# Optimization experiments

Measured on AMD Instinct MI355X. Metric: run time of the kernel, lower is better.

Reference implementation:

```python
import jax, jax.numpy as jnp
import numpy as np

B, H, S, D, KG = 1, 8, 1024, 64, 10

def setup_inputs() -> dict:
    key = jax.random.key(0)
    ks = jax.random.split(key, 16)
    n = jax.random.normal
    u = jax.random.uniform
    return {
        'Q': n(ks[0], (B, H, S, D), dtype=jnp.float32),
        'K': n(ks[1], (B, H, S, D), dtype=jnp.float32),
        'V': n(ks[2], (B, H, S, D), dtype=jnp.float32),
        'distance_matrix': u(ks[3], (B, H, S, S), dtype=jnp.float32) * 10.0,
        'energy_matrix': u(ks[4], (B, H, S, S), dtype=jnp.float32) * 5.0,
        'mask': jnp.ones((B, H, S, S), dtype=jnp.int32),
        'mu_D': n(ks[5], (KG,), dtype=jnp.float32),
        'sigma_D': u(ks[6], (KG,), dtype=jnp.float32) + 0.5,  # keep sigma positive
        'b_D': n(ks[7], (KG,), dtype=jnp.float32) * 0.1,
        'mu_E': n(ks[8], (KG,), dtype=jnp.float32),
        'sigma_E': u(ks[9], (KG,), dtype=jnp.float32) + 0.5,
        'b_E': n(ks[10], (KG,), dtype=jnp.float32) * 0.1,
        'W1': n(ks[11], (KG, KG), dtype=jnp.float32) / np.sqrt(KG),
        'b1': jnp.zeros((KG,), dtype=jnp.float32),
        'W2': n(ks[12], (1, KG), dtype=jnp.float32) / np.sqrt(KG),
        'b2': jnp.zeros((1,), dtype=jnp.float32),
    }


def _rbf_mlp_bias(x, b, mu, sigma, W1, b1, W2, b2):
    # x: [B,H,S,S] -> Gaussian RBF features over K kernels, then small MLP -> [B,H,S,S]
    z = (x[..., None] + b - mu) / sigma                      # [B,H,S,S,K]
    inv_norm = 1.0 / (jnp.sqrt(2.0 * jnp.pi) * sigma)
    psi = jnp.exp(-0.5 * z * z) * inv_norm                   # [B,H,S,S,K]
    h = jax.nn.gelu(jnp.einsum('bhijk,lk->bhijl', psi, W1) + b1, approximate=False)
    return (jnp.einsum('bhijk,lk->bhijl', h, W2) + b2)[..., 0]


def reference(Q, K, V, distance_matrix, energy_matrix, mask,
              mu_D, sigma_D, b_D, mu_E, sigma_E, b_E, W1, b1, W2, b2):
    d_model = Q.shape[-1]
    scores = jnp.einsum('bhid,bhjd->bhij', Q, K) / np.sqrt(d_model * 2)
    scores = scores + _rbf_mlp_bias(distance_matrix, b_D, mu_D, sigma_D, W1, b1, W2, b2)
    scores = scores + _rbf_mlp_bias(energy_matrix, b_E, mu_E, sigma_E, W1, b1, W2, b2)
    scores = jnp.where(mask == 0, jnp.float32(-1e9), scores)
    attn = jax.nn.softmax(scores, axis=-1)
    return jnp.einsum('bhij,bhjd->bhid', attn, V)
```

## Files before the change

kernel.cpp:

```cpp
#include <hip/hip_runtime.h>
#include <math.h>

#define Hn 8
#define Sn 1024
#define Dn 64
#define KG 10

#define TN 2048
#define RD 10.25f
#define RE 5.125f

typedef __attribute__((ext_vector_type(8))) short bf16x8;
typedef __attribute__((ext_vector_type(4))) float f32x4;
typedef _Float16 f16;
typedef __attribute__((ext_vector_type(8))) _Float16 f16x8;
typedef unsigned short u16;
typedef unsigned int u32;

__device__ inline float bf2f(u16 u) {
    union { u32 i; float f; } v;
    v.i = ((u32)u) << 16;
    return v.f;
}

__device__ inline u16 f2bf(float f) {
    union { float f; u32 i; } v;
    v.f = f;
    u32 i = v.i;
    return (u16)((i + 0x7FFFu + ((i >> 16) & 1u)) >> 16);
}

__device__ float bias_eval(float x,
                           const float* __restrict__ mu, const float* __restrict__ sg,
                           const float* __restrict__ bb,
                           const float* __restrict__ W1, const float* __restrict__ b1,
                           const float* __restrict__ W2, const float* __restrict__ b2) {
    const float inv_s2pi = 0.39894228040143267794f;
    float psi[KG];
#pragma unroll
    for (int k = 0; k < KG; k++) {
        float s = sg[k];
        float z = (x + bb[k] - mu[k]) / s;
        psi[k] = __expf(-0.5f * z * z) * (inv_s2pi / s);
    }
    float out = b2[0];
#pragma unroll
    for (int l = 0; l < KG; l++) {
        float a = b1[l];
#pragma unroll
        for (int k = 0; k < KG; k++) a += psi[k] * W1[l * KG + k];
        float g = 0.5f * a * (1.0f + erff(a * 0.70710678118654752440f));
        out += g * W2[l];
    }
    return out;
}

#define QK4 262144
#define VTN 524288

__global__ __launch_bounds__(256) void prep_kernel(
    const float* __restrict__ Q, const float* __restrict__ K, const float* __restrict__ V,
    const float* __restrict__ muD, const float* __restrict__ sgD, const float* __restrict__ bD,
    const float* __restrict__ muE, const float* __restrict__ sgE, const float* __restrict__ bE,
    const float* __restrict__ W1, const float* __restrict__ b1,
    const float* __restrict__ W2, const float* __restrict__ b2,
    u32* __restrict__ tab, u16* __restrict__ Qb, u16* __restrict__ Kb, u16* __restrict__ VTi)
{
    int id = blockIdx.x * 256 + threadIdx.x;
    if (id < 2 * TN) {
        int which = (id >= TN);
        int idx = id & (TN - 1);
        float h = (which ? RE : RD) / (float)TN;
        float x0 = idx * h;
        float v0, v1;
        if (which) {
            v0 = bias_eval(x0,     muE, sgE, bE, W1, b1, W2, b2);
            v1 = bias_eval(x0 + h, muE, sgE, bE, W1, b1, W2, b2);
        } else {
            v0 = bias_eval(x0,     muD, sgD, bD, W1, b1, W2, b2);
            v1 = bias_eval(x0 + h, muD, sgD, bD, W1, b1, W2, b2);
        }
        tab[id] = (u32)f2bf(v0) | ((u32)f2bf(v1 - v0) << 16);
    } else if (id < 2 * TN + QK4) {
        int i = id - 2 * TN;
        int arr = i >> 17;
        i &= (1 << 17) - 1;
        float4 v = ((const float4*)(arr ? K : Q))[i];
        ushort4 o;
        o.x = f2bf(v.x); o.y = f2bf(v.y); o.z = f2bf(v.z); o.w = f2bf(v.w);
        ((ushort4*)(arr ? Kb : Qb))[i] = o;
    } else if (id < 2 * TN + QK4 + VTN) {
        int g = id - (2 * TN + QK4);
        int h = g >> 16;
        int d = (g >> 10) & 63;
        int s = g & 1023;
        int t = s >> 5, q = (s >> 3) & 3, j = s & 7;
        int src_s = (t << 5) + (q << 2) + (j & 3) + ((j >> 2) << 4);
        VTi[g] = f2bf(V[(((size_t)h << 10) + src_s) * Dn + d]);
    }
}

__device__ inline float lerp_tab(const u32* __restrict__ st, float x, float invh) {
    float tf = x * invh;
    int i = (int)tf;
    i = max(0, min(i, TN - 1));
    float fr = tf - (float)i;
    u32 p = st[i];
    return fmaf(bf2f((u16)(p >> 16)), fr, bf2f((u16)p));
}

#define CB_GROUPS (Hn * 64 * 4 * 8 * 64)

__global__ __launch_bounds__(256) void bias_kernel(
    const float* __restrict__ Dm, const float* __restrict__ Em, const int* __restrict__ Mk,
    const u32* __restrict__ gtab, f16* __restrict__ Cb)
{
    __shared__ __align__(16) u32 sTab[2 * TN];
    const int tid = threadIdx.x;
    {
        const uint4* g4 = (const uint4*)gtab;
        uint4* s4 = (uint4*)sTab;
#pragma unroll
        for (int i = 0; i < 4; i++) s4[tid + 256 * i] = g4[tid + 256 * i];
    }
    __syncthreads();
    const float invhD = (float)TN / RD;
    const float invhE = (float)TN / RE;

    for (int g = blockIdx.x * 256 + tid; g < CB_GROUPS; g += gridDim.x * 256) {
        const int lane = g & 63;
        const int t    = (g >> 6) & 7;
        const int w    = (g >> 9) & 3;
        const int qb   = (g >> 11) & 63;
        const int h    = g >> 17;
        const int q    = qb * 16 + (lane & 15);
        const int k    = w * 256 + t * 32 + (lane >> 4) * 4;
        const size_t base = ((((size_t)h << 10) + q) << 10) + k;

        const float4 d0 = *(const float4*)(Dm + base);
        const float4 d1 = *(const float4*)(Dm + base + 16);
        const float4 e0 = *(const float4*)(Em + base);
        const float4 e1 = *(const float4*)(Em + base + 16);
        const int4   m0 = *(const int4*)(Mk + base);
        const int4   m1 = *(const int4*)(Mk + base + 16);

        const float dv[8] = {d0.x, d0.y, d0.z, d0.w, d1.x, d1.y, d1.z, d1.w};
        const float ev[8] = {e0.x, e0.y, e0.z, e0.w, e1.x, e1.y, e1.z, e1.w};
        const int   mv[8] = {m0.x, m0.y, m0.z, m0.w, m1.x, m1.y, m1.z, m1.w};

        f16x8 o;
#pragma unroll
        for (int j = 0; j < 8; j++) {
            float b = lerp_tab(sTab, dv[j], invhD) + lerp_tab(sTab + TN, ev[j], invhE);
            o[j] = (f16)((mv[j] == 0) ? -60000.0f : b);
        }
        ((f16x8*)Cb)[g] = o;
    }
}

__global__ __launch_bounds__(256) void attn_kernel(
    const u16* __restrict__ Qb, const u16* __restrict__ Kb, const u16* __restrict__ VTi,
    const f16* __restrict__ Cb, float* __restrict__ out)
{
    __shared__ float sO[4][16][68];
    __shared__ float sM[4][16], sL[4][16];

    const int tid  = threadIdx.x;
    const int h    = blockIdx.y;
    const int qb   = blockIdx.x;
    const int q0   = qb * 16;
    const int wave = tid >> 6;
    const int lane = tid & 63;
    const int quad = lane >> 4;
    const int l16  = lane & 15;

    const u16* Qh = Qb  + (size_t)h * Sn * Dn;
    const u16* Kh = Kb  + (size_t)h * Sn * Dn;
    const u16* Vh = VTi + (size_t)h * Dn * Sn;
    const f16x8* Cw = (const f16x8*)Cb
                    + (size_t)(((h * 64 + qb) * 4 + wave) * 8) * 64 + lane;
    const float scale = 0.08838834764831845f;

    const bf16x8 bQ0 = *(const bf16x8*)(Qh + (q0 + l16) * Dn + quad * 8);
    const bf16x8 bQ1 = *(const bf16x8*)(Qh + (q0 + l16) * Dn + 32 + quad * 8);

    f32x4 O0 = {0.f, 0.f, 0.f, 0.f}, O1 = O0, O2 = O0, O3 = O0;
    float m_run = -1e30f, l_run = 0.f;

    bf16x8 Ka[2][4];
    bf16x8 Va[2][4];
    f16x8  Ca[2];

#define LOADT(buf, tt) do {                                                   \
        const int k0_ = wave * 256 + (tt) * 32;                               \
        const u16* kr_ = Kh + (size_t)(k0_ + l16) * Dn + quad * 8;            \
        Ka[buf][0] = *(const bf16x8*)(kr_);                                   \
        Ka[buf][1] = *(const bf16x8*)(kr_ + 32);                              \
        Ka[buf][2] = *(const bf16x8*)(kr_ + 16 * Dn);                         \
        Ka[buf][3] = *(const bf16x8*)(kr_ + 16 * Dn + 32);                    \
        const u16* vr_ = Vh + k0_ + quad * 8 + (size_t)l16 * Sn;              \
        Va[buf][0] = *(const bf16x8*)(vr_);                                   \
        Va[buf][1] = *(const bf16x8*)(vr_ + 16 * Sn);                         \
        Va[buf][2] = *(const bf16x8*)(vr_ + 32 * Sn);                         \
        Va[buf][3] = *(const bf16x8*)(vr_ + 48 * Sn);                         \
        Ca[buf]    = Cw[(tt) * 64];                                           \
    } while (0)

    LOADT(0, 0);

#pragma unroll
    for (int t = 0; t < 8; t++) {
        const int cur = t & 1;
        if (t < 7) LOADT(cur ^ 1, t + 1);

        f32x4 s0 = {0.f, 0.f, 0.f, 0.f}, s1 = s0;
        s0 = __builtin_amdgcn_mfma_f32_16x16x32_bf16(Ka[cur][0], bQ0, s0, 0, 0, 0);
        s0 = __builtin_amdgcn_mfma_f32_16x16x32_bf16(Ka[cur][1], bQ1, s0, 0, 0, 0);
        s1 = __builtin_amdgcn_mfma_f32_16x16x32_bf16(Ka[cur][2], bQ0, s1, 0, 0, 0);
        s1 = __builtin_amdgcn_mfma_f32_16x16x32_bf16(Ka[cur][3], bQ1, s1, 0, 0, 0);

        float sc0[4], sc1[4];
#pragma unroll
        for (int r = 0; r < 4; r++) {
            sc0[r] = fmaf(s0[r], scale, (float)Ca[cur][r]);
            sc1[r] = fmaf(s1[r], scale, (float)Ca[cur][4 + r]);
        }

        float mloc = fmaxf(fmaxf(fmaxf(sc0[0], sc0[1]), fmaxf(sc0[2], sc0[3])),
                           fmaxf(fmaxf(sc1[0], sc1[1]), fmaxf(sc1[2], sc1[3])));
        mloc = fmaxf(mloc, __shfl_xor(mloc, 16, 64));
        mloc = fmaxf(mloc, __shfl_xor(mloc, 32, 64));

        const float mn = fmaxf(m_run, mloc);
        const float al = __expf(m_run - mn);
        m_run = mn;

        float p0[4], p1[4], ll = 0.f;
#pragma unroll
        for (int r = 0; r < 4; r++) {
            p0[r] = __expf(sc0[r] - mn);
            p1[r] = __expf(sc1[r] - mn);
            ll += p0[r] + p1[r];
        }
        ll += __shfl_xor(ll, 16, 64);
        ll += __shfl_xor(ll, 32, 64);
        l_run = l_run * al + ll;

        bf16x8 aP;
#pragma unroll
        for (int r = 0; r < 4; r++) {
            aP[r]     = (short)f2bf(p0[r]);
            aP[4 + r] = (short)f2bf(p1[r]);
        }

        const float a0 = __shfl(al, quad * 4 + 0, 64);
        const float a1 = __shfl(al, quad * 4 + 1, 64);
        const float a2 = __shfl(al, quad * 4 + 2, 64);
        const float a3 = __shfl(al, quad * 4 + 3, 64);
        O0[0] *= a0; O0[1] *= a1; O0[2] *= a2; O0[3] *= a3;
        O1[0] *= a0; O1[1] *= a1; O1[2] *= a2; O1[3] *= a3;
        O2[0] *= a0; O2[1] *= a1; O2[2] *= a2; O2[3] *= a3;
        O3[0] *= a0; O3[1] *= a1; O3[2] *= a2; O3[3] *= a3;

        O0 = __builtin_amdgcn_mfma_f32_16x16x32_bf16(aP, Va[cur][0], O0, 0, 0, 0);
        O1 = __builtin_amdgcn_mfma_f32_16x16x32_bf16(aP, Va[cur][1], O1, 0, 0, 0);
        O2 = __builtin_amdgcn_mfma_f32_16x16x32_bf16(aP, Va[cur][2], O2, 0, 0, 0);
        O3 = __builtin_amdgcn_mfma_f32_16x16x32_bf16(aP, Va[cur][3], O3, 0, 0, 0);
    }
#undef LOADT

    if (lane < 16) {
        sM[wave][lane] = m_run;
        sL[wave][lane] = l_run;
    }
#pragma unroll
    for (int r = 0; r < 4; r++) {
        sO[wave][quad * 4 + r][ 0 + l16] = O0[r];
        sO[wave][quad * 4 + r][16 + l16] = O1[r];
        sO[wave][quad * 4 + r][32 + l16] = O2[r];
        sO[wave][quad * 4 + r][48 + l16] = O3[r];
    }
    __syncthreads();

    const int row = tid >> 4;
    const int c4  = (tid & 15) * 4;
    float mg = sM[0][row];
#pragma unroll
    for (int w = 1; w < 4; w++) mg = fmaxf(mg, sM[w][row]);
    float fac[4], lg = 0.f;
#pragma unroll
    for (int w = 0; w < 4; w++) {
        fac[w] = __expf(sM[w][row] - mg);
        lg += sL[w][row] * fac[w];
    }
    const float inv = 1.0f / lg;

    float acc[4];
#pragma unroll
    for (int c = 0; c < 4; c++) {
        acc[c] = 0.f;
#pragma unroll
        for (int w = 0; w < 4; w++) acc[c] += sO[w][row][c4 + c] * fac[w];
        acc[c] *= inv;
    }
    float4 ov = {acc[0], acc[1], acc[2], acc[3]};
    *(float4*)(out + ((size_t)(h * Sn + q0 + row)) * Dn + c4) = ov;
}

extern "C" void kernel_launch(void* const* d_in, const int* in_sizes, int n_in,
                              void* d_out, int out_size, void* d_ws, size_t ws_size,
                              hipStream_t stream) {
    const float* Q    = (const float*)d_in[0];
    const float* K    = (const float*)d_in[1];
    const float* V    = (const float*)d_in[2];
    const float* Dm   = (const float*)d_in[3];
    const float* Em   = (const float*)d_in[4];
    const int*   Mask = (const int*)d_in[5];
    const float* muD  = (const float*)d_in[6];
    const float* sgD  = (const float*)d_in[7];
    const float* bD   = (const float*)d_in[8];
    const float* muE  = (const float*)d_in[9];
    const float* sgE  = (const float*)d_in[10];
    const float* bE   = (const float*)d_in[11];
    const float* W1   = (const float*)d_in[12];
    const float* b1   = (const float*)d_in[13];
    const float* W2   = (const float*)d_in[14];
    const float* b2   = (const float*)d_in[15];

    u32* tab = (u32*)d_ws;
    u16* Qb  = (u16*)((char*)d_ws + 2 * TN * 4);
    u16* Kb  = Qb + (size_t)Hn * Sn * Dn;
    u16* VTi = Kb + (size_t)Hn * Sn * Dn;
    f16* Cb  = (f16*)(VTi + (size_t)Hn * Sn * Dn);

    const int prep_threads = 2 * TN + QK4 + VTN;
    prep_kernel<<<prep_threads / 256, 256, 0, stream>>>(
        Q, K, V, muD, sgD, bD, muE, sgE, bE, W1, b1, W2, b2,
        tab, Qb, Kb, VTi);

    bias_kernel<<<2048, 256, 0, stream>>>(Dm, Em, Mask, tab, Cb);

    dim3 grid(Sn / 16, Hn);
    attn_kernel<<<grid, 256, 0, stream>>>(Qb, Kb, VTi, Cb, (float*)d_out);
}
```

Before: 185.4 us.

## Stage K/V tiles via global_load_lds and store bias in natural row-major layout

The bias kernel now writes the combined bias in plain row-major [h][q][k] order instead of an MFMA-fragment-swizzled layout, so its reads and writes are contiguous. The attention kernel drops the register double-buffered K/V/bias prefetch and instead stages each K/V tile straight into LDS with global_load_lds, waiting on vmcnt(0) before reading it back. Bias is read as two f16x4 loads per row. The intent is to cut register pressure and get coalesced traffic, but the software pipelining goes away, so each iteration waits on its own loads and memory latency is exposed.

```diff
diff --git a/kernel.cpp b/kernel.cpp
--- a/kernel.cpp
+++ b/kernel.cpp
@@ -13,6 +13,7 @@
 typedef __attribute__((ext_vector_type(8))) short bf16x8;
 typedef __attribute__((ext_vector_type(4))) float f32x4;
 typedef _Float16 f16;
+typedef __attribute__((ext_vector_type(4))) _Float16 f16x4;
 typedef __attribute__((ext_vector_type(8))) _Float16 f16x8;
 typedef unsigned short u16;
 typedef unsigned int u32;
@@ -28,6 +29,13 @@
     v.f = f;
     u32 i = v.i;
     return (u16)((i + 0x7FFFu + ((i >> 16) & 1u)) >> 16);
+}
+
+__device__ inline void stage16(const void* g, void* l) {
+    __builtin_amdgcn_global_load_lds(
+        (const __attribute__((address_space(1))) unsigned int*)g,
+        (__attribute__((address_space(3))) unsigned int*)l,
+        16, 0, 0);
 }
 
 __device__ float bias_eval(float x,
@@ -109,7 +117,7 @@
     return fmaf(bf2f((u16)(p >> 16)), fr, bf2f((u16)p));
 }
 
-#define CB_GROUPS (Hn * 64 * 4 * 8 * 64)
+#define CB_GROUPS (Hn * Sn * Sn / 8)
 
 __global__ __launch_bounds__(256) void bias_kernel(
     const float* __restrict__ Dm, const float* __restrict__ Em, const int* __restrict__ Mk,
@@ -128,21 +136,14 @@
     const float invhE = (float)TN / RE;
 
     for (int g = blockIdx.x * 256 + tid; g < CB_GROUPS; g += gridDim.x * 256) {
-        const int lane = g & 63;
-        const int t    = (g >> 6) & 7;
-        const int w    = (g >> 9) & 3;
-        const int qb   = (g >> 11) & 63;
-        const int h    = g >> 17;
-        const int q    = qb * 16 + (lane & 15);
-        const int k    = w * 256 + t * 32 + (lane >> 4) * 4;
-        const size_t base = ((((size_t)h << 10) + q) << 10) + k;
+        const size_t base = (size_t)g * 8;
 
         const float4 d0 = *(const float4*)(Dm + base);
-        const float4 d1 = *(const float4*)(Dm + base + 16);
+        const float4 d1 = *(const float4*)(Dm + base + 4);
         const float4 e0 = *(const float4*)(Em + base);
-        const float4 e1 = *(const float4*)(Em + base + 16);
+        const float4 e1 = *(const float4*)(Em + base + 4);
         const int4   m0 = *(const int4*)(Mk + base);
-        const int4   m1 = *(const int4*)(Mk + base + 16);
+        const int4   m1 = *(const int4*)(Mk + base + 4);
 
         const float dv[8] = {d0.x, d0.y, d0.z, d0.w, d1.x, d1.y, d1.z, d1.w};
         const float ev[8] = {e0.x, e0.y, e0.z, e0.w, e1.x, e1.y, e1.z, e1.w};
@@ -162,13 +163,12 @@
     const u16* __restrict__ Qb, const u16* __restrict__ Kb, const u16* __restrict__ VTi,
     const f16* __restrict__ Cb, float* __restrict__ out)
 {
-    __shared__ float sO[4][16][68];
+    __shared__ __align__(16) char sBuf[4 * 8 * 1024];
     __shared__ float sM[4][16], sL[4][16];
 
     const int tid  = threadIdx.x;
     const int h    = blockIdx.y;
-    const int qb   = blockIdx.x;
-    const int q0   = qb * 16;
+    const int q0   = blockIdx.x * 16;
     const int wave = tid >> 6;
     const int lane = tid & 63;
     const int quad = lane >> 4;
@@ -177,53 +177,57 @@
     const u16* Qh = Qb  + (size_t)h * Sn * Dn;
     const u16* Kh = Kb  + (size_t)h * Sn * Dn;
     const u16* Vh = VTi + (size_t)h * Dn * Sn;
-    const f16x8* Cw = (const f16x8*)Cb
-                    + (size_t)(((h * 64 + qb) * 4 + wave) * 8) * 64 + lane;
+    const f16* Ch = Cb  + ((size_t)h * Sn + (q0 + l16)) * Sn;
     const float scale = 0.08838834764831845f;
 
     const bf16x8 bQ0 = *(const bf16x8*)(Qh + (q0 + l16) * Dn + quad * 8);
     const bf16x8 bQ1 = *(const bf16x8*)(Qh + (q0 + l16) * Dn + 32 + quad * 8);
 
+    char* st = sBuf + wave * 8192;
+
     f32x4 O0 = {0.f, 0.f, 0.f, 0.f}, O1 = O0, O2 = O0, O3 = O0;
     float m_run = -1e30f, l_run = 0.f;
 
-    bf16x8 Ka[2][4];
-    bf16x8 Va[2][4];
-    f16x8  Ca[2];
-
-#define LOADT(buf, tt) do {                                                   \
-        const int k0_ = wave * 256 + (tt) * 32;                               \
-        const u16* kr_ = Kh + (size_t)(k0_ + l16) * Dn + quad * 8;            \
-        Ka[buf][0] = *(const bf16x8*)(kr_);                                   \
-        Ka[buf][1] = *(const bf16x8*)(kr_ + 32);                              \
-        Ka[buf][2] = *(const bf16x8*)(kr_ + 16 * Dn);                         \
-        Ka[buf][3] = *(const bf16x8*)(kr_ + 16 * Dn + 32);                    \
-        const u16* vr_ = Vh + k0_ + quad * 8 + (size_t)l16 * Sn;              \
-        Va[buf][0] = *(const bf16x8*)(vr_);                                   \
-        Va[buf][1] = *(const bf16x8*)(vr_ + 16 * Sn);                         \
-        Va[buf][2] = *(const bf16x8*)(vr_ + 32 * Sn);                         \
-        Va[buf][3] = *(const bf16x8*)(vr_ + 48 * Sn);                         \
-        Ca[buf]    = Cw[(tt) * 64];                                           \
-    } while (0)
-
-    LOADT(0, 0);
-
-#pragma unroll
     for (int t = 0; t < 8; t++) {
-        const int cur = t & 1;
-        if (t < 7) LOADT(cur ^ 1, t + 1);
+        const int k0 = wave * 256 + t * 32;
+
+        const u16* kr = Kh + (size_t)(k0 + l16) * Dn + quad * 8;
+        const u16* vr = Vh + k0 + quad * 8 + (size_t)l16 * Sn;
+        stage16(kr,               st);
+        stage16(kr + 32,          st + 1024);
+        stage16(kr + 16 * Dn,     st + 2048);
+        stage16(kr + 16 * Dn + 32,st + 3072);
+        stage16(vr,               st + 4096);
+        stage16(vr + 16 * Sn,     st + 5120);
+        stage16(vr + 32 * Sn,     st + 6144);
+        stage16(vr + 48 * Sn,     st + 7168);
+
+        const f16x4 C0 = *(const f16x4*)(Ch + k0 + quad * 4);
+        const f16x4 C1 = *(const f16x4*)(Ch + k0 + 16 + quad * 4);
+
+        asm volatile("s_waitcnt vmcnt(0)" ::: "memory");
+
+        const char* ls = st + lane * 16;
+        const bf16x8 aK00 = *(const bf16x8*)(ls);
+        const bf16x8 aK01 = *(const bf16x8*)(ls + 1024);
+        const bf16x8 aK10 = *(const bf16x8*)(ls + 2048);
+        const bf16x8 aK11 = *(const bf16x8*)(ls + 3072);
+        const bf16x8 bV0  = *(const bf16x8*)(ls + 4096);
+        const bf16x8 bV1  = *(const bf16x8*)(ls + 5120);
+        const bf16x8 bV2  = *(const bf16x8*)(ls + 6144);
+        const bf16x8 bV3  = *(const bf16x8*)(ls + 7168);
 
         f32x4 s0 = {0.f, 0.f, 0.f, 0.f}, s1 = s0;
-        s0 = __builtin_amdgcn_mfma_f32_16x16x32_bf16(Ka[cur][0], bQ0, s0, 0, 0, 0);
-        s0 = __builtin_amdgcn_mfma_f32_16x16x32_bf16(Ka[cur][1], bQ1, s0, 0, 0, 0);
-        s1 = __builtin_amdgcn_mfma_f32_16x16x32_bf16(Ka[cur][2], bQ0, s1, 0, 0, 0);
-        s1 = __builtin_amdgcn_mfma_f32_16x16x32_bf16(Ka[cur][3], bQ1, s1, 0, 0, 0);
+        s0 = __builtin_amdgcn_mfma_f32_16x16x32_bf16(aK00, bQ0, s0, 0, 0, 0);
+        s0 = __builtin_amdgcn_mfma_f32_16x16x32_bf16(aK01, bQ1, s0, 0, 0, 0);
+        s1 = __builtin_amdgcn_mfma_f32_16x16x32_bf16(aK10, bQ0, s1, 0, 0, 0);
+        s1 = __builtin_amdgcn_mfma_f32_16x16x32_bf16(aK11, bQ1, s1, 0, 0, 0);
 
         float sc0[4], sc1[4];
 #pragma unroll
         for (int r = 0; r < 4; r++) {
-            sc0[r] = fmaf(s0[r], scale, (float)Ca[cur][r]);
-            sc1[r] = fmaf(s1[r], scale, (float)Ca[cur][4 + r]);
+            sc0[r] = fmaf(s0[r], scale, (float)C0[r]);
+            sc1[r] = fmaf(s1[r], scale, (float)C1[r]);
         }
 
         float mloc = fmaxf(fmaxf(fmaxf(sc0[0], sc0[1]), fmaxf(sc0[2], sc0[3])),
@@ -262,13 +266,17 @@
         O2[0] *= a0; O2[1] *= a1; O2[2] *= a2; O2[3] *= a3;
         O3[0] *= a0; O3[1] *= a1; O3[2] *= a2; O3[3] *= a3;
 
-        O0 = __builtin_amdgcn_mfma_f32_16x16x32_bf16(aP, Va[cur][0], O0, 0, 0, 0);
-        O1 = __builtin_amdgcn_mfma_f32_16x16x32_bf16(aP, Va[cur][1], O1, 0, 0, 0);
-        O2 = __builtin_amdgcn_mfma_f32_16x16x32_bf16(aP, Va[cur][2], O2, 0, 0, 0);
-        O3 = __builtin_amdgcn_mfma_f32_16x16x32_bf16(aP, Va[cur][3], O3, 0, 0, 0);
-    }
-#undef LOADT
-
+        O0 = __builtin_amdgcn_mfma_f32_16x16x32_bf16(aP, bV0, O0, 0, 0, 0);
+        O1 = __builtin_amdgcn_mfma_f32_16x16x32_bf16(aP, bV1, O1, 0, 0, 0);
+        O2 = __builtin_amdgcn_mfma_f32_16x16x32_bf16(aP, bV2, O2, 0, 0, 0);
+        O3 = __builtin_amdgcn_mfma_f32_16x16x32_bf16(aP, bV3, O3, 0, 0, 0);
+
+        asm volatile("" ::: "memory");
+    }
+
+    __syncthreads();
+
+    float (*sO)[16][68] = (float (*)[16][68])sBuf;
     if (lane < 16) {
         sM[wave][lane] = m_run;
         sL[wave][lane] = l_run;
```

Result: no change. 185.8 us (+0.2%).
